# Performance work log

Measured on AMD Instinct MI355X. Metric: run time of the kernel, lower is better.

## Reference

```python
import jax, jax.numpy as jnp
import numpy as np

H = 128          # LSTMCell hidden size (fixed in module)
D_IN = 128       # input_dim
D_PROJ = 256     # input_layer output / LSTM input size
LAYER_NUM = 2
DA = 128
R = 8
OUT_DIM = 7
B = 256
T = 512
TS = 32          # time_steps


def _lstm_cell(h, c, x_t, W_ih, b_ih, W_hh, b_hh):
    # PyTorch LSTMCell gate order: i, f, g, o
    gates = x_t @ W_ih.T + h @ W_hh.T + (b_ih + b_hh)
    i, f, g, o = jnp.split(gates, 4, axis=-1)
    c_new = jax.nn.sigmoid(f) * c + jax.nn.sigmoid(i) * jnp.tanh(g)
    h_new = jax.nn.sigmoid(o) * jnp.tanh(c_new)
    return h_new, c_new


def _chunked_lstm(x_tbd, W_ih, b_ih, W_hh, b_hh, w_time, time_steps):
    # x_tbd: [T, B, 256]. Every `time_steps` steps, h/c are replaced by a
    # learned linear reweighting (time_w_layer) of the buffered chunk states;
    # the chunk's last emitted output is the reweighted h (as in the source).
    Tt, Bb, Dd = x_tbd.shape

    def cell_step(carry, x_t):
        h, c = carry
        h, c = _lstm_cell(h, c, x_t, W_ih, b_ih, W_hh, b_hh)
        return (h, c), (h, c)

    def chunk_step(carry, x_chunk):        # x_chunk: [ts, B, 256]
        _, (hs, cs) = jax.lax.scan(cell_step, carry, x_chunk)  # hs: [ts, B, H]
        h_new = jnp.einsum('t,tbh->bh', w_time, hs)
        c_new = jnp.einsum('t,tbh->bh', w_time, cs)
        return (h_new, c_new), hs.at[-1].set(h_new)

    n_chunks = Tt // time_steps
    x_chunks = x_tbd.reshape(n_chunks, time_steps, Bb, Dd)
    h0 = jnp.zeros((Bb, H), x_tbd.dtype)
    _, outs = jax.lax.scan(chunk_step, (h0, jnp.zeros_like(h0)), x_chunks)
    return outs.reshape(Tt, Bb, H)


def setup_inputs() -> dict:
    key = jax.random.key(0)
    ks = jax.random.split(key, 16)
    def unif(k, shape, fan_in):
        bound = 1.0 / np.sqrt(fan_in)
        return jax.random.uniform(k, shape, jnp.float32, -bound, bound)
    inp = {
        'x': jax.random.normal(ks[0], (B, T, D_IN), jnp.float32),
        'W_in': unif(ks[1], (D_PROJ, D_IN), D_IN),
        'b_in': unif(ks[2], (D_PROJ,), D_IN),
        'W_ih': unif(ks[3], (4 * H, D_PROJ), H),
        'b_ih': unif(ks[4], (4 * H,), H),
        'W_hh': unif(ks[5], (4 * H, H), H),
        'b_hh': unif(ks[6], (4 * H,), H),
        'w_time': unif(ks[7], (TS,), TS),
        'W_a1': unif(ks[8], (DA, 2 * H), 2 * H),
        'b_a1': unif(ks[9], (DA,), 2 * H),
        'W_a2': unif(ks[10], (R, DA), DA),
        'W_out': unif(ks[11], (OUT_DIM, 2 * H * R), 2 * H * R),
        'b_out': unif(ks[12], (OUT_DIM,), 2 * H * R),
        'length': jax.random.randint(ks[13], (B,), T // 2, T + 1),
        'batch_size': B,
        'time_steps': TS,
        'r': R,
    }
    return inp


def reference(x, W_in, b_in, W_ih, b_ih, W_hh, b_hh, w_time, W_a1, b_a1,
              W_a2, W_out, b_out, length, batch_size, time_steps, r):
    Bb, Tt, _ = x.shape
    out = x @ W_in.T + b_in                       # [B, T, 256]
    for _ in range(LAYER_NUM):                    # shared LSTM weights per source
        inp = jnp.transpose(out, (1, 0, 2))       # [T, B, 256]
        out1 = _chunked_lstm(inp, W_ih, b_ih, W_hh, b_hh, w_time, time_steps)
        out2 = _chunked_lstm(inp[::-1], W_ih, b_ih, W_hh, b_hh, w_time, time_steps)
        # NOTE: backward outputs are NOT re-reversed (faithful to source)
        out = jnp.transpose(jnp.concatenate([out1, out2], axis=-1), (1, 0, 2))
    # attention (dropout = identity at eval)
    pot = jnp.tanh(out @ W_a1.T + b_a1) @ W_a2.T  # [B, T, r]
    mask = (jnp.arange(Tt)[None, :] < length[:, None])[:, :, None]
    logits = jnp.where(mask, pot, -jnp.inf)
    weight = jnp.where(mask, jax.nn.softmax(logits, axis=1), 0.0)  # [B, T, r]
    wT = jnp.transpose(weight, (0, 2, 1))          # [B, r, T]
    pooled = jnp.einsum('brt,bth->brh', wT, out).reshape(Bb, -1)   # [B, r*256]
    out_final = jax.nn.log_softmax(pooled @ W_out.T + b_out, axis=1)
    sw = jnp.sqrt(wT)
    gram = jnp.einsum('brt,bst->brs', sw, sw)      # [B, r, r]
    penalty = jnp.sum((gram - 1.0) ** 2)           # oneMat is all-ones
    return out_final, penalty
```

## Files before the change

### kernel.cpp

```cpp
#include <hip/hip_runtime.h>
#include <math.h>

namespace {

constexpr int Bb = 256, Tt = 512, Dp = 256, Hh = 128, G = 512;
constexpr int M = Tt * Bb;

typedef __attribute__((ext_vector_type(8))) short short8v;
typedef __attribute__((ext_vector_type(4))) float f32x4;

__device__ __forceinline__ float sigf(float x) {
  return __builtin_amdgcn_rcpf(1.0f + __expf(-x));
}
__device__ __forceinline__ float tanhfast(float x) {
  const float e = __expf(2.0f * x);
  return 1.0f - 2.0f * __builtin_amdgcn_rcpf(e + 1.0f);
}
__device__ __forceinline__ float b2f(unsigned short u) {
  return __uint_as_float((unsigned int)u << 16);
}
__device__ __forceinline__ unsigned short f2b(float f) {
  unsigned int u = __float_as_uint(f);
  u += 0x7FFFu + ((u >> 16) & 1u);
  return (unsigned short)(u >> 16);
}
__device__ __forceinline__ unsigned int pack2(float a, float b) {
  return (unsigned int)f2b(a) | ((unsigned int)f2b(b) << 16);
}
__device__ __forceinline__ void block_sync_lds() {
  __builtin_amdgcn_sched_barrier(0);
  asm volatile("s_waitcnt lgkmcnt(0)" ::: "memory");
  __builtin_amdgcn_s_barrier();
  __builtin_amdgcn_sched_barrier(0);
}

template<int K, int SWAP, int TANH, typename AT, typename CT>
__global__ __launch_bounds__(256) void mgemm_k(const AT* __restrict__ A,
    const float* __restrict__ W, const float* __restrict__ bias1,
    const float* __restrict__ bias2, CT* __restrict__ C, int N) {
  constexpr int NK = K / 64;
  __shared__ unsigned short aLds[2][8192];
  __shared__ unsigned short wLds[2][8192];
  const int tid = threadIdx.x;
  const int lane = tid & 63;
  const int wave = tid >> 6;
  const int wm = wave >> 1, wn = wave & 1;
  const int m0 = blockIdx.y * 128, n0 = blockIdx.x * 128;

  const int srow = tid >> 1;
  const int skc = tid & 1;
  int am;
  if constexpr (SWAP) { const int m = m0 + srow; am = (m & 255) * Tt + (m >> 8); }
  else am = m0 + srow;

  uint4 ra[4];
  float4 raf[4][2];
  float4 rw[4][2];

  auto loadA = [&](int kb) {
    const int kbase = kb * 64 + skc * 32;
    if constexpr (sizeof(AT) == 2) {
      const unsigned short* src = reinterpret_cast<const unsigned short*>(A) + (size_t)am * K + kbase;
#pragma unroll
      for (int q = 0; q < 4; ++q) ra[q] = *reinterpret_cast<const uint4*>(src + q * 8);
    } else {
      const float* src = reinterpret_cast<const float*>(A) + (size_t)am * K + kbase;
#pragma unroll
      for (int q = 0; q < 4; ++q) {
        raf[q][0] = *reinterpret_cast<const float4*>(src + q * 8);
        raf[q][1] = *reinterpret_cast<const float4*>(src + q * 8 + 4);
      }
    }
  };
  auto loadW = [&](int kb) {
    const int kbase = kb * 64 + skc * 32;
    const float* src = W + (size_t)(n0 + srow) * K + kbase;
#pragma unroll
    for (int q = 0; q < 4; ++q) {
      rw[q][0] = *reinterpret_cast<const float4*>(src + q * 8);
      rw[q][1] = *reinterpret_cast<const float4*>(src + q * 8 + 4);
    }
  };
  auto writeS = [&](int buf) {
    const int base = (skc * 8 + (srow >> 4)) * 64 + (srow & 15);
#pragma unroll
    for (int q = 0; q < 4; ++q) {
      const int slot = base + q * 16;
      if constexpr (sizeof(AT) == 2) {
        *reinterpret_cast<uint4*>(&aLds[buf][slot * 8]) = ra[q];
      } else {
        uint4 p;
        p.x = pack2(raf[q][0].x, raf[q][0].y); p.y = pack2(raf[q][0].z, raf[q][0].w);
        p.z = pack2(raf[q][1].x, raf[q][1].y); p.w = pack2(raf[q][1].z, raf[q][1].w);
        *reinterpret_cast<uint4*>(&aLds[buf][slot * 8]) = p;
      }
      uint4 pw;
      pw.x = pack2(rw[q][0].x, rw[q][0].y); pw.y = pack2(rw[q][0].z, rw[q][0].w);
      pw.z = pack2(rw[q][1].x, rw[q][1].y); pw.w = pack2(rw[q][1].z, rw[q][1].w);
      *reinterpret_cast<uint4*>(&wLds[buf][slot * 8]) = pw;
    }
  };

  f32x4 acc[4][4] = {};
  int cur = 0;
  loadA(0); loadW(0); writeS(0);
  __syncthreads();
  for (int kb = 0; kb < NK; ++kb) {
    const bool more = (kb + 1 < NK);
    if (more) { loadA(kb + 1); loadW(kb + 1); }
#pragma unroll
    for (int kc = 0; kc < 2; ++kc) {
      short8v af[4], bfr[4];
#pragma unroll
      for (int i = 0; i < 4; ++i)
        af[i] = *reinterpret_cast<const short8v*>(
            &aLds[cur][((kc * 8 + wm * 4 + i) * 64 + lane) * 8]);
#pragma unroll
      for (int j = 0; j < 4; ++j)
        bfr[j] = *reinterpret_cast<const short8v*>(
            &wLds[cur][((kc * 8 + wn * 4 + j) * 64 + lane) * 8]);
#pragma unroll
      for (int i = 0; i < 4; ++i)
#pragma unroll
        for (int j = 0; j < 4; ++j)
          acc[i][j] = __builtin_amdgcn_mfma_f32_16x16x32_bf16(af[i], bfr[j], acc[i][j], 0, 0, 0);
    }
    if (more) writeS(cur ^ 1);
    __syncthreads();
    cur ^= 1;
  }
#pragma unroll
  for (int j = 0; j < 4; ++j) {
    const int gn = n0 + wn * 64 + j * 16 + (lane & 15);
    float bv = bias1[gn];
    if (bias2) bv += bias2[gn];
#pragma unroll
    for (int i = 0; i < 4; ++i) {
      const int gmb = m0 + wm * 64 + i * 16 + ((lane >> 4) << 2);
#pragma unroll
      for (int r = 0; r < 4; ++r) {
        float v = acc[i][j][r] + bv;
        if (TANH) v = tanhfast(v);
        const size_t oidx = (size_t)(gmb + r) * N + gn;
        if constexpr (sizeof(CT) == 2) C[oidx] = f2b(v); else C[oidx] = v;
      }
    }
  }
}

__global__ __launch_bounds__(512, 2) void lstm_k(const unsigned short* __restrict__ P,
    const float* __restrict__ Whh, const float* __restrict__ wtime,
    unsigned short* __restrict__ Y) {
  const int tid = threadIdx.x;
  const int lane = tid & 63;
  const int w = tid >> 6;
  const int u = lane & 15;
  const int q = lane >> 4;
  const int dir = blockIdx.x >> 7;
  const int b0 = (blockIdx.x & 127) * 2;

  __shared__ unsigned short hbuf[2][2048];
  __shared__ unsigned int pgbuf[2][512];
  __shared__ unsigned short histb[4096];
  __shared__ float wts[32];

  short8v bfrag[4][4];
#pragma unroll
  for (int gt = 0; gt < 4; ++gt) {
    const int col = gt * 128 + w * 16 + u;
#pragma unroll
    for (int ks = 0; ks < 4; ++ks) {
      const int k0 = ks * 32 + q * 8;
      const float4 w0 = *reinterpret_cast<const float4*>(Whh + (size_t)col * 128 + k0);
      const float4 w1 = *reinterpret_cast<const float4*>(Whh + (size_t)col * 128 + k0 + 4);
      short8v f;
      f[0] = (short)f2b(w0.x); f[1] = (short)f2b(w0.y);
      f[2] = (short)f2b(w0.z); f[3] = (short)f2b(w0.w);
      f[4] = (short)f2b(w1.x); f[5] = (short)f2b(w1.y);
      f[6] = (short)f2b(w1.z); f[7] = (short)f2b(w1.w);
      bfrag[gt][ks] = f;
    }
  }

  for (int i = tid; i < 2048; i += 512) { hbuf[0][i] = 0; hbuf[1][i] = 0; }
  if (tid < 32) wts[tid] = wtime[tid];
  const unsigned int* P32 = reinterpret_cast<const unsigned int*>(P);
  const int prow = tid >> 8, pword = tid & 255;
  const size_t pthread = (size_t)(b0 + prow) * 256 + pword;
  const ptrdiff_t dstep = (dir ? -(ptrdiff_t)1 : (ptrdiff_t)1) * (ptrdiff_t)(Bb * 256);
  unsigned int np_h1 = 0, np_h2 = 0;
  {
    const int t0 = dir ? (Tt - 1) : 0;
    pgbuf[0][tid] = P32[(size_t)t0 * Bb * 256 + pthread];
    const int t1 = dir ? (Tt - 2) : 1;
    np_h1 = P32[(size_t)t1 * Bb * 256 + pthread];
    const int t2 = dir ? (Tt - 3) : 2;
    np_h2 = P32[(size_t)t2 * Bb * 256 + pthread];
  }
  ptrdiff_t poff = (ptrdiff_t)((size_t)(dir ? (Tt - 4) : 3) * Bb * 256 + pthread);
  const int r_own = q & 1;
  const int colh = w * 16 + u;
  float c_st = 0.f, ha = 0.f, ca = 0.f;
  __syncthreads();

  auto body = [&](int s, int cur) {
    unsigned int np_new = 0;
    if (s < Tt - 3) np_new = P32[poff];
    short8v afrag[4];
#pragma unroll
    for (int ks = 0; ks < 4; ++ks)
      afrag[ks] = *reinterpret_cast<const short8v*>(&hbuf[cur][(ks * 4 + q) * 128 + u * 8]);
    f32x4 gacc[4];
#pragma unroll
    for (int gt = 0; gt < 4; ++gt) {
      f32x4 acc = {0.f, 0.f, 0.f, 0.f};
#pragma unroll
      for (int ks = 0; ks < 4; ++ks)
        acc = __builtin_amdgcn_mfma_f32_16x16x32_bf16(afrag[ks], bfrag[gt][ks], acc, 0, 0, 0);
      gacc[gt] = acc;
    }
    if (s + 1 < Tt) pgbuf[cur ^ 1][tid] = np_h1;
    if (lane < 32) {
      const float wt = wts[s & 31];
      float g4[4];
#pragma unroll
      for (int gt = 0; gt < 4; ++gt) {
        const unsigned int pw = pgbuf[cur][r_own * 256 + gt * 64 + (colh >> 1)];
        const unsigned short pb = (colh & 1) ? (unsigned short)(pw >> 16)
                                             : (unsigned short)(pw & 0xFFFF);
        g4[gt] = gacc[gt][0] + b2f(pb);
      }
      float cs = sigf(g4[1]) * c_st + sigf(g4[0]) * tanhfast(g4[2]);
      float hn = sigf(g4[3]) * tanhfast(cs);
      ha += wt * hn;
      ca += wt * cs;
      if ((s & 31) == 31) { hn = ha; cs = ca; ha = 0.f; ca = 0.f; }
      c_st = cs;
      const unsigned short hb = f2b(hn);
      hbuf[cur ^ 1][(colh >> 3) * 128 + r_own * 32 + (colh & 7)] = hb;
      histb[((s & 15) * 2 + r_own) * 128 + colh] = hb;
    }
    if ((s & 7) == 0 && s) {
      const int k = tid >> 6, r2 = (tid >> 5) & 1, c4 = (tid & 31) * 4;
      const int bs = s - 8;
      const uint2 v = *reinterpret_cast<const uint2*>(
          &histb[(((bs + k) & 15) * 2 + r2) * 128 + c4]);
      *reinterpret_cast<uint2*>(
          &Y[((size_t)(bs + k) * Bb + b0 + r2) * Dp + dir * Hh + c4]) = v;
    }
    block_sync_lds();
    np_h1 = np_h2;
    np_h2 = np_new;
    poff += dstep;
  };

  for (int s = 0; s < Tt; s += 2) {
    body(s, 0);
    body(s + 1, 1);
  }
  {
    const int k = tid >> 6, r2 = (tid >> 5) & 1, c4 = (tid & 31) * 4;
    const int bs = Tt - 8;
    const uint2 v = *reinterpret_cast<const uint2*>(
        &histb[(((bs + k) & 15) * 2 + r2) * 128 + c4]);
    *reinterpret_cast<uint2*>(
        &Y[((size_t)(bs + k) * Bb + b0 + r2) * Dp + dir * Hh + c4]) = v;
  }
}

__global__ __launch_bounds__(256) void pot_k(const float* __restrict__ tmp,
    const float* __restrict__ Wa2, float* __restrict__ pot) {
  const int tid = threadIdx.x;
  const int row = blockIdx.x * 32 + (tid >> 3);
  const int r = tid & 7;
  __shared__ float w2[8 * 129];
  for (int i = tid; i < 1024; i += 256) w2[(i >> 7) * 129 + (i & 127)] = Wa2[i];
  __syncthreads();
  float acc = 0.f;
  const float* tr = tmp + (size_t)row * 128;
#pragma unroll
  for (int k4 = 0; k4 < 32; ++k4) {
    const float4 tv = *reinterpret_cast<const float4*>(tr + k4 * 4);
    acc += tv.x * w2[r * 129 + k4 * 4 + 0];
    acc += tv.y * w2[r * 129 + k4 * 4 + 1];
    acc += tv.z * w2[r * 129 + k4 * 4 + 2];
    acc += tv.w * w2[r * 129 + k4 * 4 + 3];
  }
  pot[(size_t)row * 8 + r] = acc;
}

__global__ __launch_bounds__(256) void softmax_k(const float* __restrict__ pot,
    const int* __restrict__ length, float* __restrict__ Wt) {
  const int b = blockIdx.x >> 3, r = blockIdx.x & 7;
  const int tid = threadIdx.x;
  const int len = length[b];
  __shared__ float rbuf[4];
  const int t1 = tid, t2 = tid + 256;
  const float x1 = (t1 < len) ? pot[((size_t)t1 * Bb + b) * 8 + r] : -INFINITY;
  const float x2 = (t2 < len) ? pot[((size_t)t2 * Bb + b) * 8 + r] : -INFINITY;
  float m = fmaxf(x1, x2);
#pragma unroll
  for (int off = 32; off >= 1; off >>= 1) m = fmaxf(m, __shfl_xor(m, off));
  if ((tid & 63) == 0) rbuf[tid >> 6] = m;
  __syncthreads();
  m = fmaxf(fmaxf(rbuf[0], rbuf[1]), fmaxf(rbuf[2], rbuf[3]));
  const float e1 = (t1 < len) ? __expf(x1 - m) : 0.f;
  const float e2 = (t2 < len) ? __expf(x2 - m) : 0.f;
  float ssum = e1 + e2;
#pragma unroll
  for (int off = 32; off >= 1; off >>= 1) ssum += __shfl_xor(ssum, off);
  __syncthreads();
  if ((tid & 63) == 0) rbuf[tid >> 6] = ssum;
  __syncthreads();
  ssum = rbuf[0] + rbuf[1] + rbuf[2] + rbuf[3];
  const float inv = 1.0f / ssum;
  float* wrow = Wt + ((size_t)b * 8 + r) * Tt;
  wrow[t1] = e1 * inv;
  wrow[t2] = e2 * inv;
}

__global__ __launch_bounds__(256) void pool_k(const unsigned short* __restrict__ Y,
    const float* __restrict__ Wt, const float* __restrict__ Wout,
    const float* __restrict__ bout, float* __restrict__ outF,
    float* __restrict__ penpart) {
  const int b = blockIdx.x;
  const int tid = threadIdx.x;
  __shared__ float ws[8 * 513];
  __shared__ float pooled[2048];
  __shared__ float red[256];
  __shared__ float lg[8];
  for (int i = tid; i < 4096; i += 256) ws[(i >> 9) * 513 + (i & 511)] = Wt[(size_t)b * 4096 + i];
  __syncthreads();
  float acc[8] = {};
  for (int t = 0; t < Tt; ++t) {
    const float y = b2f(Y[((size_t)t * Bb + b) * Dp + tid]);
#pragma unroll
    for (int r = 0; r < 8; ++r) acc[r] += ws[r * 513 + t] * y;
  }
#pragma unroll
  for (int r = 0; r < 8; ++r) pooled[r * 256 + tid] = acc[r];
  __syncthreads();
  for (int o = 0; o < 7; ++o) {
    float p = 0.f;
    for (int j = tid; j < 2048; j += 256) p += pooled[j] * Wout[(size_t)o * 2048 + j];
    red[tid] = p;
    __syncthreads();
    for (int st = 128; st >= 1; st >>= 1) {
      if (tid < st) red[tid] += red[tid + st];
      __syncthreads();
    }
    if (tid == 0) lg[o] = red[0] + bout[o];
    __syncthreads();
  }
  if (tid == 0) {
    float mx = lg[0];
    for (int o = 1; o < 7; ++o) mx = fmaxf(mx, lg[o]);
    float ssum = 0.f;
    for (int o = 0; o < 7; ++o) ssum += __expf(lg[o] - mx);
    const float lse = mx + __logf(ssum);
    for (int o = 0; o < 7; ++o) outF[b * 7 + o] = lg[o] - lse;
  }
  for (int i = tid; i < 4096; i += 256) {
    const int rr = i >> 9, t = i & 511;
    ws[rr * 513 + t] = sqrtf(ws[rr * 513 + t]);
  }
  __syncthreads();
  float pp = 0.f;
  if (tid < 64) {
    const int rr = tid >> 3, ssi = tid & 7;
    float g = 0.f;
    for (int t = 0; t < Tt; ++t) g += ws[rr * 513 + t] * ws[ssi * 513 + t];
    const float d = g - 1.0f;
    pp = d * d;
  }
  red[tid] = pp;
  __syncthreads();
  for (int st = 128; st >= 1; st >>= 1) {
    if (tid < st) red[tid] += red[tid + st];
    __syncthreads();
  }
  if (tid == 0) penpart[b] = red[0];
}

__global__ __launch_bounds__(256) void penred_k(const float* __restrict__ penpart,
                                                float* __restrict__ outp) {
  const int tid = threadIdx.x;
  __shared__ float red[256];
  red[tid] = penpart[tid];
  __syncthreads();
  for (int st = 128; st >= 1; st >>= 1) {
    if (tid < st) red[tid] += red[tid + st];
    __syncthreads();
  }
  if (tid == 0) outp[0] = red[0];
}

}

extern "C" void kernel_launch(void* const* d_in, const int* in_sizes, int n_in,
                              void* d_out, int out_size, void* d_ws, size_t ws_size,
                              hipStream_t stream) {
  (void)in_sizes; (void)n_in; (void)out_size;
  const float* x     = (const float*)d_in[0];
  const float* W_in  = (const float*)d_in[1];
  const float* b_in  = (const float*)d_in[2];
  const float* W_ih  = (const float*)d_in[3];
  const float* b_ih  = (const float*)d_in[4];
  const float* W_hh  = (const float*)d_in[5];
  const float* b_hh  = (const float*)d_in[6];
  const float* wtime = (const float*)d_in[7];
  const float* W_a1  = (const float*)d_in[8];
  const float* b_a1  = (const float*)d_in[9];
  const float* W_a2  = (const float*)d_in[10];
  const float* W_out = (const float*)d_in[11];
  const float* b_out = (const float*)d_in[12];
  const int*   length= (const int*)d_in[13];
  float* outF = (float*)d_out;

  typedef unsigned short bf16;
  char* ws = (char*)d_ws;
  size_t off = 0;
  auto alloc = [&](size_t bytes) {
    void* p = ws + off; off += (bytes + 255) & ~(size_t)255; return p;
  };
  bf16*  act  = (bf16*)alloc((size_t)M * 256 * 2);
  bf16*  Pg   = (bf16*)alloc((size_t)M * 512 * 2);
  float* pot  = (float*)alloc((size_t)M * 8 * 4);
  float* Wt   = (float*)alloc((size_t)Bb * 8 * Tt * 4);
  float* penp = (float*)alloc(Bb * 4);
  float* tmpA = (float*)Pg;

  if (ws_size < off) return;

  const dim3 blk(256);
  mgemm_k<128, 1, 0, float, bf16><<<dim3(2, M / 128), blk, 0, stream>>>(x, W_in, b_in, nullptr, act, 256);
  mgemm_k<256, 0, 0, bf16, bf16><<<dim3(4, M / 128), blk, 0, stream>>>(act, W_ih, b_ih, b_hh, Pg, 512);
  lstm_k<<<dim3(256), dim3(512), 0, stream>>>(Pg, W_hh, wtime, act);
  mgemm_k<256, 0, 0, bf16, bf16><<<dim3(4, M / 128), blk, 0, stream>>>(act, W_ih, b_ih, b_hh, Pg, 512);
  lstm_k<<<dim3(256), dim3(512), 0, stream>>>(Pg, W_hh, wtime, act);
  mgemm_k<256, 0, 1, bf16, float><<<dim3(1, M / 128), blk, 0, stream>>>(act, W_a1, b_a1, nullptr, tmpA, 128);
  pot_k<<<dim3(M / 32), blk, 0, stream>>>(tmpA, W_a2, pot);
  softmax_k<<<dim3(Bb * 8), blk, 0, stream>>>(pot, length, Wt);
  pool_k<<<dim3(Bb), blk, 0, stream>>>(act, Wt, W_out, b_out, outF, penp);
  penred_k<<<dim3(1), blk, 0, stream>>>(penp, outF + Bb * 7);
}
```

Before: 1.050 ms.

## Pre-convert weights to bf16, stage GEMM tiles via global_load_lds, fuse pot projection

Weights and the input x are converted to bf16 once by small conversion kernels, with x transposed to time-major at the same time. The GEMM then stages A/W tiles straight into LDS with global_load_lds instead of register round-trips and packing. The attention GEMM now fuses tanh and the W_a2 projection via an extra MFMA pass in its epilogue, which removes the fp32 temporary and the separate pot kernel. This adds four extra launches and a bf16 rounding of the tanh output before the second projection.

```diff
diff --git a/kernel.cpp b/kernel.cpp
--- a/kernel.cpp
+++ b/kernel.cpp
@@ -26,6 +26,11 @@
 }
 __device__ __forceinline__ unsigned int pack2(float a, float b) {
   return (unsigned int)f2b(a) | ((unsigned int)f2b(b) << 16);
+}
+__device__ __forceinline__ void gload16(const unsigned short* g, unsigned short* l) {
+  __builtin_amdgcn_global_load_lds(
+      (const __attribute__((address_space(1))) unsigned int*)g,
+      (__attribute__((address_space(3))) unsigned int*)l, 16, 0, 0);
 }
 __device__ __forceinline__ void block_sync_lds() {
   __builtin_amdgcn_sched_barrier(0);
@@ -34,115 +39,143 @@
   __builtin_amdgcn_sched_barrier(0);
 }
 
-template<int K, int SWAP, int TANH, typename AT, typename CT>
-__global__ __launch_bounds__(256) void mgemm_k(const AT* __restrict__ A,
-    const float* __restrict__ W, const float* __restrict__ bias1,
-    const float* __restrict__ bias2, CT* __restrict__ C, int N) {
+__global__ __launch_bounds__(256) void wconv_k(const float* __restrict__ src,
+                                               unsigned short* __restrict__ dst) {
+  const int i = (blockIdx.x * 256 + threadIdx.x) * 4;
+  const float4 v = *reinterpret_cast<const float4*>(src + i);
+  uint2 o; o.x = pack2(v.x, v.y); o.y = pack2(v.z, v.w);
+  *reinterpret_cast<uint2*>(dst + i) = o;
+}
+
+__global__ __launch_bounds__(256) void xconv_k(const float* __restrict__ x,
+                                               unsigned short* __restrict__ out) {
+  const int tid = threadIdx.x;
+  const int m = blockIdx.x * 8 + (tid >> 5);
+  const int t = m >> 8, b = m & 255;
+  const int c4 = (tid & 31) * 4;
+  const float4 v = *reinterpret_cast<const float4*>(x + ((size_t)b * Tt + t) * 128 + c4);
+  uint2 o; o.x = pack2(v.x, v.y); o.y = pack2(v.z, v.w);
+  *reinterpret_cast<uint2*>(out + (size_t)m * 128 + c4) = o;
+}
+
+template<int K, int POT, typename CT>
+__global__ __launch_bounds__(256) void mgemm_k(const unsigned short* __restrict__ A,
+    const unsigned short* __restrict__ W, const float* __restrict__ bias1,
+    const float* __restrict__ bias2, const float* __restrict__ Wa2,
+    CT* __restrict__ C, int N) {
   constexpr int NK = K / 64;
-  __shared__ unsigned short aLds[2][8192];
-  __shared__ unsigned short wLds[2][8192];
+  __shared__ unsigned short smem[32768];
+  unsigned short* aLds = smem;
+  unsigned short* wLds = smem + 16384;
   const int tid = threadIdx.x;
   const int lane = tid & 63;
   const int wave = tid >> 6;
   const int wm = wave >> 1, wn = wave & 1;
   const int m0 = blockIdx.y * 128, n0 = blockIdx.x * 128;
-
-  const int srow = tid >> 1;
-  const int skc = tid & 1;
-  int am;
-  if constexpr (SWAP) { const int m = m0 + srow; am = (m & 255) * Tt + (m >> 8); }
-  else am = m0 + srow;
-
-  uint4 ra[4];
-  float4 raf[4][2];
-  float4 rw[4][2];
-
-  auto loadA = [&](int kb) {
-    const int kbase = kb * 64 + skc * 32;
-    if constexpr (sizeof(AT) == 2) {
-      const unsigned short* src = reinterpret_cast<const unsigned short*>(A) + (size_t)am * K + kbase;
-#pragma unroll
-      for (int q = 0; q < 4; ++q) ra[q] = *reinterpret_cast<const uint4*>(src + q * 8);
-    } else {
-      const float* src = reinterpret_cast<const float*>(A) + (size_t)am * K + kbase;
-#pragma unroll
-      for (int q = 0; q < 4; ++q) {
-        raf[q][0] = *reinterpret_cast<const float4*>(src + q * 8);
-        raf[q][1] = *reinterpret_cast<const float4*>(src + q * 8 + 4);
-      }
+  const int lrow = lane & 15, lk8 = (lane >> 4) * 8;
+
+  const unsigned short* Ab = A + (size_t)(m0 + lrow) * K + lk8;
+  const unsigned short* Wb = W + (size_t)(n0 + lrow) * K + lk8;
+
+  auto stage = [&](int buf, int kb) {
+#pragma unroll
+    for (int i = 0; i < 4; ++i) {
+      const int c = wave * 4 + i, f = c & 7, kc = c >> 3;
+      const size_t go = (size_t)(f * 16) * K + kb * 64 + kc * 32;
+      gload16(Ab + go, &aLds[buf * 8192 + c * 512]);
+      gload16(Wb + go, &wLds[buf * 8192 + c * 512]);
     }
   };
-  auto loadW = [&](int kb) {
-    const int kbase = kb * 64 + skc * 32;
-    const float* src = W + (size_t)(n0 + srow) * K + kbase;
-#pragma unroll
-    for (int q = 0; q < 4; ++q) {
-      rw[q][0] = *reinterpret_cast<const float4*>(src + q * 8);
-      rw[q][1] = *reinterpret_cast<const float4*>(src + q * 8 + 4);
-    }
-  };
-  auto writeS = [&](int buf) {
-    const int base = (skc * 8 + (srow >> 4)) * 64 + (srow & 15);
-#pragma unroll
-    for (int q = 0; q < 4; ++q) {
-      const int slot = base + q * 16;
-      if constexpr (sizeof(AT) == 2) {
-        *reinterpret_cast<uint4*>(&aLds[buf][slot * 8]) = ra[q];
-      } else {
-        uint4 p;
-        p.x = pack2(raf[q][0].x, raf[q][0].y); p.y = pack2(raf[q][0].z, raf[q][0].w);
-        p.z = pack2(raf[q][1].x, raf[q][1].y); p.w = pack2(raf[q][1].z, raf[q][1].w);
-        *reinterpret_cast<uint4*>(&aLds[buf][slot * 8]) = p;
-      }
-      uint4 pw;
-      pw.x = pack2(rw[q][0].x, rw[q][0].y); pw.y = pack2(rw[q][0].z, rw[q][0].w);
-      pw.z = pack2(rw[q][1].x, rw[q][1].y); pw.w = pack2(rw[q][1].z, rw[q][1].w);
-      *reinterpret_cast<uint4*>(&wLds[buf][slot * 8]) = pw;
-    }
-  };
 
   f32x4 acc[4][4] = {};
+  stage(0, 0);
+  __syncthreads();
   int cur = 0;
-  loadA(0); loadW(0); writeS(0);
-  __syncthreads();
   for (int kb = 0; kb < NK; ++kb) {
-    const bool more = (kb + 1 < NK);
-    if (more) { loadA(kb + 1); loadW(kb + 1); }
+    if (kb + 1 < NK) stage(cur ^ 1, kb + 1);
 #pragma unroll
     for (int kc = 0; kc < 2; ++kc) {
       short8v af[4], bfr[4];
 #pragma unroll
       for (int i = 0; i < 4; ++i)
         af[i] = *reinterpret_cast<const short8v*>(
-            &aLds[cur][((kc * 8 + wm * 4 + i) * 64 + lane) * 8]);
+            &aLds[cur * 8192 + ((kc * 8 + wm * 4 + i) * 64 + lane) * 8]);
 #pragma unroll
       for (int j = 0; j < 4; ++j)
         bfr[j] = *reinterpret_cast<const short8v*>(
-            &wLds[cur][((kc * 8 + wn * 4 + j) * 64 + lane) * 8]);
+            &wLds[cur * 8192 + ((kc * 8 + wn * 4 + j) * 64 + lane) * 8]);
 #pragma unroll
       for (int i = 0; i < 4; ++i)
 #pragma unroll
         for (int j = 0; j < 4; ++j)
           acc[i][j] = __builtin_amdgcn_mfma_f32_16x16x32_bf16(af[i], bfr[j], acc[i][j], 0, 0, 0);
     }
-    if (more) writeS(cur ^ 1);
     __syncthreads();
     cur ^= 1;
   }
-#pragma unroll
-  for (int j = 0; j < 4; ++j) {
-    const int gn = n0 + wn * 64 + j * 16 + (lane & 15);
-    float bv = bias1[gn];
-    if (bias2) bv += bias2[gn];
-#pragma unroll
-    for (int i = 0; i < 4; ++i) {
-      const int gmb = m0 + wm * 64 + i * 16 + ((lane >> 4) << 2);
-#pragma unroll
-      for (int r = 0; r < 4; ++r) {
-        float v = acc[i][j][r] + bv;
-        if (TANH) v = tanhfast(v);
-        const size_t oidx = (size_t)(gmb + r) * N + gn;
-        if constexpr (sizeof(CT) == 2) C[oidx] = f2b(v); else C[oidx] = v;
+
+  if constexpr (POT) {
+    unsigned short* pt = smem;
+#pragma unroll
+    for (int j = 0; j < 4; ++j) {
+      const int coln = wn * 64 + j * 16 + (lane & 15);
+      const float bv = bias1[coln];
+#pragma unroll
+      for (int i = 0; i < 4; ++i) {
+        const int rown = wm * 64 + i * 16 + ((lane >> 4) << 2);
+#pragma unroll
+        for (int r = 0; r < 4; ++r)
+          pt[(rown + r) * 136 + coln] = f2b(tanhfast(acc[i][j][r] + bv));
+      }
+    }
+    __syncthreads();
+    short8v wfr[4];
+#pragma unroll
+    for (int ks = 0; ks < 4; ++ks) {
+      short8v f = {0, 0, 0, 0, 0, 0, 0, 0};
+      if (lrow < 8) {
+        const float* src = Wa2 + lrow * 128 + ks * 32 + lk8;
+        const float4 a = *reinterpret_cast<const float4*>(src);
+        const float4 b = *reinterpret_cast<const float4*>(src + 4);
+        f[0] = (short)f2b(a.x); f[1] = (short)f2b(a.y);
+        f[2] = (short)f2b(a.z); f[3] = (short)f2b(a.w);
+        f[4] = (short)f2b(b.x); f[5] = (short)f2b(b.y);
+        f[6] = (short)f2b(b.z); f[7] = (short)f2b(b.w);
+      }
+      wfr[ks] = f;
+    }
+    float* pot = reinterpret_cast<float*>(C);
+#pragma unroll
+    for (int ff = 0; ff < 2; ++ff) {
+      const int fr = wave * 2 + ff;
+      f32x4 pacc = {0.f, 0.f, 0.f, 0.f};
+#pragma unroll
+      for (int ks = 0; ks < 4; ++ks) {
+        const short8v af = *reinterpret_cast<const short8v*>(
+            &pt[(fr * 16 + lrow) * 136 + ks * 32 + lk8]);
+        pacc = __builtin_amdgcn_mfma_f32_16x16x32_bf16(af, wfr[ks], pacc, 0, 0, 0);
+      }
+      if ((lane & 15) < 8) {
+#pragma unroll
+        for (int r = 0; r < 4; ++r)
+          pot[(size_t)(m0 + fr * 16 + ((lane >> 4) << 2) + r) * 8 + (lane & 15)] = pacc[r];
+      }
+    }
+  } else {
+#pragma unroll
+    for (int j = 0; j < 4; ++j) {
+      const int gn = n0 + wn * 64 + j * 16 + (lane & 15);
+      float bv = bias1[gn];
+      if (bias2) bv += bias2[gn];
+#pragma unroll
+      for (int i = 0; i < 4; ++i) {
+        const int gmb = m0 + wm * 64 + i * 16 + ((lane >> 4) << 2);
+#pragma unroll
+        for (int r = 0; r < 4; ++r) {
+          const float v = acc[i][j][r] + bv;
+          const size_t oidx = (size_t)(gmb + r) * N + gn;
+          if constexpr (sizeof(CT) == 2) C[oidx] = f2b(v); else C[oidx] = v;
+        }
       }
     }
   }
@@ -266,27 +299,6 @@
     *reinterpret_cast<uint2*>(
         &Y[((size_t)(bs + k) * Bb + b0 + r2) * Dp + dir * Hh + c4]) = v;
   }
-}
-
-__global__ __launch_bounds__(256) void pot_k(const float* __restrict__ tmp,
-    const float* __restrict__ Wa2, float* __restrict__ pot) {
-  const int tid = threadIdx.x;
-  const int row = blockIdx.x * 32 + (tid >> 3);
-  const int r = tid & 7;
-  __shared__ float w2[8 * 129];
-  for (int i = tid; i < 1024; i += 256) w2[(i >> 7) * 129 + (i & 127)] = Wa2[i];
-  __syncthreads();
-  float acc = 0.f;
-  const float* tr = tmp + (size_t)row * 128;
-#pragma unroll
-  for (int k4 = 0; k4 < 32; ++k4) {
-    const float4 tv = *reinterpret_cast<const float4*>(tr + k4 * 4);
-    acc += tv.x * w2[r * 129 + k4 * 4 + 0];
-    acc += tv.y * w2[r * 129 + k4 * 4 + 1];
-    acc += tv.z * w2[r * 129 + k4 * 4 + 2];
-    acc += tv.w * w2[r * 129 + k4 * 4 + 3];
-  }
-  pot[(size_t)row * 8 + r] = acc;
 }
 
 __global__ __launch_bounds__(256) void softmax_k(const float* __restrict__ pot,
@@ -425,21 +437,27 @@
   };
   bf16*  act  = (bf16*)alloc((size_t)M * 256 * 2);
   bf16*  Pg   = (bf16*)alloc((size_t)M * 512 * 2);
+  bf16*  xb   = (bf16*)alloc((size_t)M * 128 * 2);
   float* pot  = (float*)alloc((size_t)M * 8 * 4);
   float* Wt   = (float*)alloc((size_t)Bb * 8 * Tt * 4);
   float* penp = (float*)alloc(Bb * 4);
-  float* tmpA = (float*)Pg;
+  bf16*  Wihb = (bf16*)alloc(512 * 256 * 2);
+  bf16*  Winb = (bf16*)alloc(256 * 128 * 2);
+  bf16*  Wa1b = (bf16*)alloc(128 * 256 * 2);
 
   if (ws_size < off) return;
 
   const dim3 blk(256);
-  mgemm_k<128, 1, 0, float, bf16><<<dim3(2, M / 128), blk, 0, stream>>>(x, W_in, b_in, nullptr, act, 256);
-  mgemm_k<256, 0, 0, bf16, bf16><<<dim3(4, M / 128), blk, 0, stream>>>(act, W_ih, b_ih, b_hh, Pg, 512);
+  wconv_k<<<dim3(32),  blk, 0, stream>>>(W_in, Winb);
+  wconv_k<<<dim3(128), blk, 0, stream>>>(W_ih, Wihb);
+  wconv_k<<<dim3(32),  blk, 0, stream>>>(W_a1, Wa1b);
+  xconv_k<<<dim3(M / 8), blk, 0, stream>>>(x, xb);
+  mgemm_k<128, 0, bf16><<<dim3(2, M / 128), blk, 0, stream>>>(xb, Winb, b_in, nullptr, nullptr, act, 256);
+  mgemm_k<256, 0, bf16><<<dim3(4, M / 128), blk, 0, stream>>>(act, Wihb, b_ih, b_hh, nullptr, Pg, 512);
   lstm_k<<<dim3(256), dim3(512), 0, stream>>>(Pg, W_hh, wtime, act);
-  mgemm_k<256, 0, 0, bf16, bf16><<<dim3(4, M / 128), blk, 0, stream>>>(act, W_ih, b_ih, b_hh, Pg, 512);
+  mgemm_k<256, 0, bf16><<<dim3(4, M / 128), blk, 0, stream>>>(act, Wihb, b_ih, b_hh, nullptr, Pg, 512);
   lstm_k<<<dim3(256), dim3(512), 0, stream>>>(Pg, W_hh, wtime, act);
-  mgemm_k<256, 0, 1, bf16, float><<<dim3(1, M / 128), blk, 0, stream>>>(act, W_a1, b_a1, nullptr, tmpA, 128);
-  pot_k<<<dim3(M / 32), blk, 0, stream>>>(tmpA, W_a2, pot);
+  mgemm_k<256, 1, float><<<dim3(1, M / 128), blk, 0, stream>>>(act, Wa1b, b_a1, nullptr, W_a2, pot, 128);
   softmax_k<<<dim3(Bb * 8), blk, 0, stream>>>(pot, length, Wt);
   pool_k<<<dim3(Bb), blk, 0, stream>>>(act, Wt, W_out, b_out, outF, penp);
   penred_k<<<dim3(1), blk, 0, stream>>>(penp, outF + Bb * 7);
```

Result: faster. 898.0 us (-14.5%).
